# Kernel tuning notes

Measured on AMD Instinct MI355X. Metric: run time of the kernel, lower is better.

The kernel has to match this reference:

```python
import jax, jax.numpy as jnp
import numpy as np
from math import sqrt

N_BLOCKS = 15
N_HIDDEN = 128
N_BINARY = 10
NODE_DIM = 16
EDGE_DIM = 8
N_NODES = 20000
N_EDGES = 640000


def _norm_std(h):
    # x / x.std(-1, keepdim=True).detach()  (torch std is unbiased, ddof=1)
    s = jax.lax.stop_gradient(jnp.std(h, axis=-1, keepdims=True, ddof=1))
    return h / s


def setup_inputs() -> dict:
    key = jax.random.key(0)
    ks = jax.random.split(key, 16)
    inp = {
        "x": jax.random.uniform(ks[0], (N_NODES, NODE_DIM), jnp.float32),
        "edge_index": jax.random.randint(ks[1], (2, N_EDGES), 0, N_NODES, jnp.int32),
        "edge_attr": jax.random.uniform(ks[2], (N_EDGES, EDGE_DIM), jnp.float32),
        "embed_W": jax.random.normal(ks[3], (NODE_DIM, N_HIDDEN), jnp.float32) / sqrt(NODE_DIM),
        "embed_b": jax.random.normal(ks[4], (N_HIDDEN,), jnp.float32) * 0.02,
        "edge_W": jax.random.normal(ks[5], (N_BLOCKS, EDGE_DIM, N_HIDDEN), jnp.float32) / sqrt(EDGE_DIM),
        "edge_b": jax.random.normal(ks[6], (N_BLOCKS, N_HIDDEN), jnp.float32) * 0.02,
        "W1": jax.random.normal(ks[7], (N_BLOCKS, N_HIDDEN, N_HIDDEN), jnp.float32) / sqrt(N_HIDDEN),
        "b1": jax.random.normal(ks[8], (N_BLOCKS, N_HIDDEN), jnp.float32) * 0.02,
        "W2": jax.random.normal(ks[9], (N_BLOCKS, N_HIDDEN, N_HIDDEN), jnp.float32) / sqrt(N_HIDDEN),
        "b2": jax.random.normal(ks[10], (N_BLOCKS, N_HIDDEN), jnp.float32) * 0.02,
        "W3": jax.random.normal(ks[11], (N_BLOCKS, N_HIDDEN, N_HIDDEN), jnp.float32) / sqrt(N_HIDDEN),
        "b3": jax.random.normal(ks[12], (N_BLOCKS, N_HIDDEN), jnp.float32) * 0.02,
        "out_W": jax.random.normal(ks[13], (N_HIDDEN, N_BINARY), jnp.float32) / sqrt(N_HIDDEN),
        "out_b": jax.random.normal(ks[14], (N_BINARY,), jnp.float32) * 0.02,
    }
    return inp


def reference(x, edge_index, edge_attr, embed_W, embed_b, edge_W, edge_b,
              W1, b1, W2, b2, W3, b3, out_W, out_b):
    n_nodes = x.shape[0]
    src, dst = edge_index[0], edge_index[1]

    x = jnp.log(x + 1.0)                    # [N, node_dim]
    ea = jnp.log(edge_attr + 1.0)           # [E, edge_dim]
    h = x @ embed_W + embed_b               # [N, H]

    def block(h, p):
        eW, eb, w1, c1, w2, c2, w3, c3 = p
        x2 = _norm_std(h)
        e = ea @ eW + eb                    # per-block edge embedding [E, H]
        msg = jax.nn.relu(x2[src] + e)      # GINE message [E, H]
        agg = jax.ops.segment_sum(msg, dst, num_segments=n_nodes)  # [N, H]
        z = x2 + agg                        # (1 + eps) * x2 + aggr, eps=0
        z = jax.nn.relu(z @ w1 + c1)
        z = jax.nn.relu(z @ w2 + c2)
        z = z @ w3 + c3
        y = _norm_std(z)
        return h + y, None

    h, _ = jax.lax.scan(block, h, (edge_W, edge_b, W1, b1, W2, b2, W3, b3))

    h = h / sqrt(N_BLOCKS)
    logits = h @ out_W + out_b              # [N, N_BINARY]
    scale = 2.0 ** jnp.arange(N_BINARY, dtype=jnp.float32)  # fixed buffer
    return jnp.sum(logits * scale, axis=-1, keepdims=True)  # [N, 1]
```

## Files before the change

### kernel.cpp

```cpp
#include <hip/hip_runtime.h>
#include <hip/hip_bf16.h>
#include <hip/hip_fp16.h>

#define N_NODES 20000
#define N_EDGES 640000
#define N_HIDDEN 128
#define EDGE_DIM 8
#define NODE_DIM 16
#define N_BLOCKS 15
#define N_BINARY 10

typedef __attribute__((ext_vector_type(8))) _Float16 f16x8;
typedef __attribute__((ext_vector_type(4))) float f32x4;
typedef unsigned int uint;
typedef unsigned short ushort;

union U2H {
  uint u;
  __half2 h;
};
static __device__ __forceinline__ __half2 u2h2(uint u) {
  U2H c; c.u = u; return c.h;
}
static __device__ __forceinline__ ushort f2h_bits(float f) {
  union { _Float16 h; ushort u; } c;
  c.h = (_Float16)f;
  return c.u;
}

__global__ void k_embed(const float* __restrict__ x, const float* __restrict__ eW,
                        const float* __restrict__ ebias, float* __restrict__ h,
                        uint* __restrict__ x2p) {
  int wid = (blockIdx.x * blockDim.x + threadIdx.x) >> 6;
  int lane = threadIdx.x & 63;
  if (wid >= N_NODES) return;
  float xl[NODE_DIM];
#pragma unroll
  for (int k = 0; k < NODE_DIM; k++) xl[k] = logf(x[wid * NODE_DIM + k] + 1.0f);
  int c0 = lane, c1 = lane + 64;
  float h0 = ebias[c0], h1 = ebias[c1];
#pragma unroll
  for (int k = 0; k < NODE_DIM; k++) {
    h0 += xl[k] * eW[k * N_HIDDEN + c0];
    h1 += xl[k] * eW[k * N_HIDDEN + c1];
  }
  float ss = h0 + h1, s2 = h0 * h0 + h1 * h1;
#pragma unroll
  for (int m = 1; m < 64; m <<= 1) {
    ss += __shfl_xor(ss, m);
    s2 += __shfl_xor(s2, m);
  }
  float var = (s2 - ss * ss * (1.0f / 128.0f)) * (1.0f / 127.0f);
  float inv = 1.0f / sqrtf(var);
  size_t o = (size_t)wid * N_HIDDEN;
  h[o + c0] = h0;
  h[o + c1] = h1;
  uint pk = (uint)f2h_bits(h0 * inv) | ((uint)f2h_bits(h1 * inv) << 16);
  x2p[(size_t)wid * 64 + lane] = pk;
}

__global__ void k_count(const int* __restrict__ ei, int* __restrict__ deg,
                        int* __restrict__ rnk) {
  int e = blockIdx.x * blockDim.x + threadIdx.x;
  if (e < N_EDGES) rnk[e] = atomicAdd(&deg[ei[N_EDGES + e]], 1);
}

__global__ __launch_bounds__(1024) void k_scan(const int* __restrict__ deg,
                                               int* __restrict__ off) {
  __shared__ int wsum[16];
  int t = threadIdx.x;
  int lane = t & 63, w = t >> 6;
  int base = t * 20;
  int loc[20];
  int s = 0;
#pragma unroll
  for (int i = 0; i < 20; i++) {
    int idx = base + i;
    int d = (idx < N_NODES) ? deg[idx] : 0;
    loc[i] = s;
    s += d;
  }
  int incl = s;
#pragma unroll
  for (int m = 1; m < 64; m <<= 1) {
    int o = __shfl_up(incl, m);
    if (lane >= m) incl += o;
  }
  if (lane == 63) wsum[w] = incl;
  __syncthreads();
  if (w == 0) {
    int xv = (lane < 16) ? wsum[lane] : 0;
#pragma unroll
    for (int m = 1; m < 16; m <<= 1) {
      int o = __shfl_up(xv, m);
      if (lane >= m) xv += o;
    }
    if (lane < 16) wsum[lane] = xv;
  }
  __syncthreads();
  int woff = (w == 0) ? 0 : wsum[w - 1];
  int texcl = woff + incl - s;
#pragma unroll
  for (int i = 0; i < 20; i++) {
    int idx = base + i;
    if (idx < N_NODES) off[idx] = texcl + loc[i];
  }
  if (t == 0) off[N_NODES] = wsum[15];
}

__global__ void k_permute(const int* __restrict__ ei, const float* __restrict__ eattr,
                          const int* __restrict__ off, const int* __restrict__ rnk,
                          uint* __restrict__ srcoff, _Float16* __restrict__ ea_h) {
  int e = blockIdx.x * blockDim.x + threadIdx.x;
  if (e >= N_EDGES) return;
  int d = ei[N_EDGES + e];
  int pos = off[d] + rnk[e];
  srcoff[pos] = (uint)ei[e] * 64u;
  const float4* ap = (const float4*)(eattr + (size_t)e * 8);
  float4 a0 = ap[0], a1 = ap[1];
  f16x8 r;
  r[0] = (_Float16)logf(a0.x + 1.0f);
  r[1] = (_Float16)logf(a0.y + 1.0f);
  r[2] = (_Float16)logf(a0.z + 1.0f);
  r[3] = (_Float16)logf(a0.w + 1.0f);
  r[4] = (_Float16)logf(a1.x + 1.0f);
  r[5] = (_Float16)logf(a1.y + 1.0f);
  r[6] = (_Float16)logf(a1.z + 1.0f);
  r[7] = (_Float16)logf(a1.w + 1.0f);
  *(f16x8*)(ea_h + (size_t)pos * 8) = r;
}

__global__ void k_prep_w(const float* __restrict__ W1, const float* __restrict__ W2,
                         const float* __restrict__ W3, _Float16* __restrict__ Wt) {
  __shared__ _Float16 t[128][130];
  int m = blockIdx.x;
  int blk = m / 3, layer = m % 3;
  const float* src = (layer == 0 ? W1 : layer == 1 ? W2 : W3) + (size_t)blk * 16384;
  int tid = threadIdx.x;
  for (int idx = tid; idx < 16384; idx += 256) {
    int k = idx >> 7, n = idx & 127;
    t[k][n] = (_Float16)src[idx];
  }
  __syncthreads();
  _Float16* dst = Wt + (size_t)m * 16384;
  if (layer == 0) {
    for (int idx = tid; idx < 16384; idx += 256) {
      int n = idx >> 7, p = idx & 127;
      int k = (p >> 1) + 64 * (p & 1);
      dst[idx] = t[k][n];
    }
  } else {
    for (int idx = tid; idx < 16384; idx += 256) {
      int n = idx >> 7, k = idx & 127;
      dst[idx] = t[k][n];
    }
  }
}

__global__ __launch_bounds__(256) void k_block(
    const int* __restrict__ off, const uint* __restrict__ srcoff,
    const _Float16* __restrict__ ea_h, const uint* __restrict__ x2in,
    const float* __restrict__ eW, const float* __restrict__ ebias,
    const _Float16* __restrict__ Wt, const float* __restrict__ b1,
    const float* __restrict__ b2, const float* __restrict__ b3,
    float* __restrict__ h, uint* __restrict__ x2out) {
  __shared__ __align__(16) uint lzU[16 * 68];
  __shared__ float zf[16][132];
  int tid = threadIdx.x;
  int w = tid >> 6, lane = tid & 63;
  int l15 = lane & 15, g = lane >> 4;
  int g0 = blockIdx.x * 16;

  __half2 w0pk[4], w1pk[4];
#pragma unroll
  for (int j = 0; j < 4; j++) {
    w0pk[j] = __floats2half2_rn(eW[(2 * j) * N_HIDDEN + lane],
                                eW[(2 * j + 1) * N_HIDDEN + lane]);
    w1pk[j] = __floats2half2_rn(eW[(2 * j) * N_HIDDEN + lane + 64],
                                eW[(2 * j + 1) * N_HIDDEN + lane + 64]);
  }
  __half2 bb01 = __floats2half2_rn(ebias[lane], ebias[lane + 64]);

#define EDGE_COMPUTE(EV, UA)                                                   \
  {                                                                            \
    __half2 pA = __hmul2(u2h2((EV).x), w0pk[0]);                               \
    pA = __hfma2(u2h2((EV).y), w0pk[1], pA);                                   \
    pA = __hfma2(u2h2((EV).z), w0pk[2], pA);                                   \
    pA = __hfma2(u2h2((EV).w), w0pk[3], pA);                                   \
    __half2 pB = __hmul2(u2h2((EV).x), w1pk[0]);                               \
    pB = __hfma2(u2h2((EV).y), w1pk[1], pB);                                   \
    pB = __hfma2(u2h2((EV).z), w1pk[2], pB);                                   \
    pB = __hfma2(u2h2((EV).w), w1pk[3], pB);                                   \
    __half v0 = __hadd(__low2half(pA), __high2half(pA));                       \
    __half v1 = __hadd(__low2half(pB), __high2half(pB));                       \
    __half2 mm = __hadd2(__halves2half2(v0, v1), __hadd2(u2h2(UA), bb01));     \
    acc0 += fmaxf(__low2float(mm), 0.f);                                       \
    acc1 += fmaxf(__high2float(mm), 0.f);                                      \
  }
#define SLOAD4(SO, EV, EE)                                                     \
  {                                                                            \
    int eU_ = __builtin_amdgcn_readfirstlane(EE);                              \
    SO[0] = srcoff[eU_];                                                       \
    SO[1] = srcoff[eU_ + 1];                                                   \
    SO[2] = srcoff[eU_ + 2];                                                   \
    SO[3] = srcoff[eU_ + 3];                                                   \
    const uint4* ep_ = (const uint4*)(ea_h + (size_t)eU_ * 8);                 \
    EV[0] = ep_[0];                                                            \
    EV[1] = ep_[1];                                                            \
    EV[2] = ep_[2];                                                            \
    EV[3] = ep_[3];                                                            \
  }
#define GATHER4(UA, SO)                                                        \
  {                                                                            \
    UA[0] = x2in[SO[0] + lane];                                                \
    UA[1] = x2in[SO[1] + lane];                                                \
    UA[2] = x2in[SO[2] + lane];                                                \
    UA[3] = x2in[SO[3] + lane];                                                \
  }
#define COMP4(EV, UA)                                                          \
  {                                                                            \
    EDGE_COMPUTE(EV[0], UA[0]);                                                \
    EDGE_COMPUTE(EV[1], UA[1]);                                                \
    EDGE_COMPUTE(EV[2], UA[2]);                                                \
    EDGE_COMPUTE(EV[3], UA[3]);                                                \
  }

  for (int i = 0; i < 4; ++i) {
    int nl = w * 4 + i;
    int nU = __builtin_amdgcn_readfirstlane(g0 + nl);
    int eBeg = off[nU], eEnd = off[nU + 1];
    float acc0 = 0.f, acc1 = 0.f;

    uint soA[4], soB[4], uaA[4], uaB[4];
    uint4 evA[4], evB[4];
    int n4 = (eEnd - eBeg) >> 2;
    int e = eBeg;
    if (n4 > 0) {
      SLOAD4(soA, evA, e);
      SLOAD4(soB, evB, e + 4);
      GATHER4(uaA, soA);
      int gg = 0;
      for (; gg + 1 < n4; gg += 2) {
        GATHER4(uaB, soB);
        COMP4(evA, uaA);
        SLOAD4(soA, evA, e + 8);
        GATHER4(uaA, soA);
        COMP4(evB, uaB);
        SLOAD4(soB, evB, e + 12);
        e += 8;
      }
      if (gg < n4) {
        COMP4(evA, uaA);
        e += 4;
      }
    }
    for (; e < eEnd; ++e) {
      int eU = __builtin_amdgcn_readfirstlane(e);
      uint so = srcoff[eU];
      uint4 ev = *(const uint4*)(ea_h + (size_t)eU * 8);
      uint ua = x2in[so + lane];
      EDGE_COMPUTE(ev, ua);
    }

    uint xp = x2in[(uint)nU * 64u + lane];
    float z0 = __low2float(u2h2(xp)) + acc0;
    float z1 = __high2float(u2h2(xp)) + acc1;
    lzU[nl * 68 + lane] = (uint)f2h_bits(z0) | ((uint)f2h_bits(z1) << 16);
  }
#undef COMP4
#undef GATHER4
#undef SLOAD4
#undef EDGE_COMPUTE
  __syncthreads();

  f32x4 acc[2];
  f16x8 a[4];
  ushort* lzS = (ushort*)lzU;

#pragma unroll
  for (int kk = 0; kk < 4; kk++)
    a[kk] = *(const f16x8*)&lzU[l15 * 68 + kk * 16 + g * 4];
  __syncthreads();
#pragma unroll
  for (int c = 0; c < 2; c++) {
    float bv = b1[32 * w + c * 16 + l15];
    acc[c] = (f32x4){bv, bv, bv, bv};
  }
#pragma unroll
  for (int c = 0; c < 2; c++) {
    int col = 32 * w + c * 16 + l15;
#pragma unroll
    for (int kk = 0; kk < 4; kk++) {
      f16x8 bf = *(const f16x8*)(Wt + (size_t)col * 128 + kk * 32 + g * 8);
      acc[c] = __builtin_amdgcn_mfma_f32_16x16x32_f16(a[kk], bf, acc[c], 0, 0, 0);
    }
  }
#pragma unroll
  for (int c = 0; c < 2; c++)
#pragma unroll
    for (int r = 0; r < 4; r++)
      lzS[(4 * g + r) * 136 + 32 * w + c * 16 + l15] =
          f2h_bits(fmaxf(acc[c][r], 0.f));
  __syncthreads();

#pragma unroll
  for (int kk = 0; kk < 4; kk++)
    a[kk] = *(const f16x8*)&lzU[l15 * 68 + kk * 16 + g * 4];
  __syncthreads();
#pragma unroll
  for (int c = 0; c < 2; c++) {
    float bv = b2[32 * w + c * 16 + l15];
    acc[c] = (f32x4){bv, bv, bv, bv};
  }
  {
    const _Float16* W2t = Wt + 16384;
#pragma unroll
    for (int c = 0; c < 2; c++) {
      int col = 32 * w + c * 16 + l15;
#pragma unroll
      for (int kk = 0; kk < 4; kk++) {
        f16x8 bf = *(const f16x8*)(W2t + (size_t)col * 128 + kk * 32 + g * 8);
        acc[c] = __builtin_amdgcn_mfma_f32_16x16x32_f16(a[kk], bf, acc[c], 0, 0, 0);
      }
    }
  }
#pragma unroll
  for (int c = 0; c < 2; c++)
#pragma unroll
    for (int r = 0; r < 4; r++)
      lzS[(4 * g + r) * 136 + 32 * w + c * 16 + l15] =
          f2h_bits(fmaxf(acc[c][r], 0.f));
  __syncthreads();

#pragma unroll
  for (int kk = 0; kk < 4; kk++)
    a[kk] = *(const f16x8*)&lzU[l15 * 68 + kk * 16 + g * 4];
#pragma unroll
  for (int c = 0; c < 2; c++) {
    float bv = b3[32 * w + c * 16 + l15];
    acc[c] = (f32x4){bv, bv, bv, bv};
  }
  {
    const _Float16* W3t = Wt + 32768;
#pragma unroll
    for (int c = 0; c < 2; c++) {
      int col = 32 * w + c * 16 + l15;
#pragma unroll
      for (int kk = 0; kk < 4; kk++) {
        f16x8 bf = *(const f16x8*)(W3t + (size_t)col * 128 + kk * 32 + g * 8);
        acc[c] = __builtin_amdgcn_mfma_f32_16x16x32_f16(a[kk], bf, acc[c], 0, 0, 0);
      }
    }
  }
#pragma unroll
  for (int c = 0; c < 2; c++)
#pragma unroll
    for (int r = 0; r < 4; r++)
      zf[4 * g + r][32 * w + c * 16 + l15] = acc[c][r];
  __syncthreads();

#pragma unroll
  for (int i = 0; i < 4; ++i) {
    int nl = w * 4 + i;
    int n = g0 + nl;
    float z0 = zf[nl][lane], z1 = zf[nl][lane + 64];
    float ss = z0 + z1, s2 = z0 * z0 + z1 * z1;
#pragma unroll
    for (int m = 1; m < 64; m <<= 1) {
      ss += __shfl_xor(ss, m);
      s2 += __shfl_xor(s2, m);
    }
    float inv = 1.0f / sqrtf((s2 - ss * ss * (1.0f / 128.0f)) * (1.0f / 127.0f));
    size_t o = (size_t)n * 128;
    float h0 = h[o + lane] + z0 * inv;
    float h1 = h[o + lane + 64] + z1 * inv;
    float ts = h0 + h1, t2 = h0 * h0 + h1 * h1;
#pragma unroll
    for (int m = 1; m < 64; m <<= 1) {
      ts += __shfl_xor(ts, m);
      t2 += __shfl_xor(t2, m);
    }
    float inv2 = 1.0f / sqrtf((t2 - ts * ts * (1.0f / 128.0f)) * (1.0f / 127.0f));
    h[o + lane] = h0;
    h[o + lane + 64] = h1;
    uint pk = (uint)f2h_bits(h0 * inv2) | ((uint)f2h_bits(h1 * inv2) << 16);
    x2out[(uint)n * 64u + lane] = pk;
  }
}

__global__ void k_out(const float* __restrict__ h, const float* __restrict__ oW,
                      const float* __restrict__ ob, float* __restrict__ out) {
  int wid = (blockIdx.x * blockDim.x + threadIdx.x) >> 6;
  int lane = threadIdx.x & 63;
  if (wid >= N_NODES) return;
  int c0 = lane, c1 = lane + 64;
  float w0 = 0.f, w1 = 0.f, bsum = 0.f;
#pragma unroll
  for (int j = 0; j < N_BINARY; j++) {
    float sc = (float)(1 << j);
    w0 += oW[c0 * N_BINARY + j] * sc;
    w1 += oW[c1 * N_BINARY + j] * sc;
    bsum += ob[j] * sc;
  }
  size_t o = (size_t)wid * 128;
  float v = h[o + c0] * w0 + h[o + c1] * w1;
#pragma unroll
  for (int m = 1; m < 64; m <<= 1) v += __shfl_xor(v, m);
  if (lane == 0) out[wid] = v * (1.0f / sqrtf(15.0f)) + bsum;
}

extern "C" void kernel_launch(void* const* d_in, const int* in_sizes, int n_in,
                              void* d_out, int out_size, void* d_ws, size_t ws_size,
                              hipStream_t stream) {
  const float* x = (const float*)d_in[0];
  const int* ei = (const int*)d_in[1];
  const float* eattr = (const float*)d_in[2];
  const float* embW = (const float*)d_in[3];
  const float* embB = (const float*)d_in[4];
  const float* edgeW = (const float*)d_in[5];
  const float* edgeB = (const float*)d_in[6];
  const float* W1 = (const float*)d_in[7];
  const float* b1 = (const float*)d_in[8];
  const float* W2 = (const float*)d_in[9];
  const float* b2 = (const float*)d_in[10];
  const float* W3 = (const float*)d_in[11];
  const float* b3 = (const float*)d_in[12];
  const float* outW = (const float*)d_in[13];
  const float* outB = (const float*)d_in[14];
  float* out = (float*)d_out;

  char* base = (char*)d_ws;
  size_t o = 0;
  auto carve = [&](size_t bytes) {
    size_t start = o;
    o = (start + bytes + 255) & ~(size_t)255;
    return (void*)(base + start);
  };
  int* deg = (int*)carve(N_NODES * sizeof(int));
  int* off = (int*)carve((N_NODES + 1) * sizeof(int));
  int* rnk = (int*)carve(N_EDGES * sizeof(int));
  uint* srcoff = (uint*)carve((N_EDGES + 16) * sizeof(uint));
  _Float16* ea_h = (_Float16*)carve((size_t)(N_EDGES + 16) * EDGE_DIM * 2);
  uint* x2a = (uint*)carve((size_t)N_NODES * 64 * sizeof(uint));
  uint* x2b = (uint*)carve((size_t)N_NODES * 64 * sizeof(uint));
  float* h = (float*)carve((size_t)N_NODES * N_HIDDEN * sizeof(float));
  _Float16* Wt = (_Float16*)carve((size_t)45 * 16384 * 2);

  hipMemsetAsync(deg, 0, N_NODES * sizeof(int), stream);
  hipMemsetAsync(srcoff + N_EDGES, 0, 16 * sizeof(uint), stream);
  k_embed<<<N_NODES / 4, 256, 0, stream>>>(x, embW, embB, h, x2a);
  k_count<<<(N_EDGES + 255) / 256, 256, 0, stream>>>(ei, deg, rnk);
  k_scan<<<1, 1024, 0, stream>>>(deg, off);
  k_permute<<<(N_EDGES + 255) / 256, 256, 0, stream>>>(ei, eattr, off, rnk, srcoff, ea_h);
  k_prep_w<<<45, 256, 0, stream>>>(W1, W2, W3, Wt);

  for (int b = 0; b < N_BLOCKS; b++) {
    const uint* x2i = (b & 1) ? x2b : x2a;
    uint* x2o = (b & 1) ? x2a : x2b;
    k_block<<<N_NODES / 16, 256, 0, stream>>>(
        off, srcoff, ea_h, x2i, edgeW + (size_t)b * EDGE_DIM * N_HIDDEN,
        edgeB + (size_t)b * N_HIDDEN, Wt + (size_t)b * 3 * 16384,
        b1 + (size_t)b * N_HIDDEN, b2 + (size_t)b * N_HIDDEN,
        b3 + (size_t)b * N_HIDDEN, h, x2o);
  }
  k_out<<<N_NODES / 4, 256, 0, stream>>>(h, outW, outB, out);
}
```

Measured before the change: 957.2 us.

## Use eight waves per block to halve per-wave node and column work

Each k_block workgroup now launches 512 threads (8 waves) instead of 256. Each wave gathers edges for 2 nodes instead of 4 and computes one 16-column MFMA tile per layer instead of two. The goal is more concurrent waves hiding the latency of the irregular gather, plus shorter serial chains per wave. In exchange, the register budget per thread is tighter under the 512 launch bound, and each workgroup has more waves meeting at every barrier.

```diff
diff --git a/kernel.cpp b/kernel.cpp
--- a/kernel.cpp
+++ b/kernel.cpp
@@ -157,7 +157,7 @@
   }
 }
 
-__global__ __launch_bounds__(256) void k_block(
+__global__ __launch_bounds__(512) void k_block(
     const int* __restrict__ off, const uint* __restrict__ srcoff,
     const _Float16* __restrict__ ea_h, const uint* __restrict__ x2in,
     const float* __restrict__ eW, const float* __restrict__ ebias,
@@ -225,8 +225,8 @@
     EDGE_COMPUTE(EV[3], UA[3]);                                                \
   }
 
-  for (int i = 0; i < 4; ++i) {
-    int nl = w * 4 + i;
+  for (int i = 0; i < 2; ++i) {
+    int nl = w * 2 + i;
     int nU = __builtin_amdgcn_readfirstlane(g0 + nl);
     int eBeg = off[nU], eEnd = off[nU + 1];
     float acc0 = 0.f, acc1 = 0.f;
@@ -273,95 +273,68 @@
 #undef EDGE_COMPUTE
   __syncthreads();
 
-  f32x4 acc[2];
+  f32x4 acc;
   f16x8 a[4];
   ushort* lzS = (ushort*)lzU;
+  int col = 16 * w + l15;
 
 #pragma unroll
   for (int kk = 0; kk < 4; kk++)
     a[kk] = *(const f16x8*)&lzU[l15 * 68 + kk * 16 + g * 4];
   __syncthreads();
-#pragma unroll
-  for (int c = 0; c < 2; c++) {
-    float bv = b1[32 * w + c * 16 + l15];
-    acc[c] = (f32x4){bv, bv, bv, bv};
-  }
-#pragma unroll
-  for (int c = 0; c < 2; c++) {
-    int col = 32 * w + c * 16 + l15;
+  {
+    float bv = b1[col];
+    acc = (f32x4){bv, bv, bv, bv};
 #pragma unroll
     for (int kk = 0; kk < 4; kk++) {
       f16x8 bf = *(const f16x8*)(Wt + (size_t)col * 128 + kk * 32 + g * 8);
-      acc[c] = __builtin_amdgcn_mfma_f32_16x16x32_f16(a[kk], bf, acc[c], 0, 0, 0);
-    }
-  }
-#pragma unroll
-  for (int c = 0; c < 2; c++)
-#pragma unroll
-    for (int r = 0; r < 4; r++)
-      lzS[(4 * g + r) * 136 + 32 * w + c * 16 + l15] =
-          f2h_bits(fmaxf(acc[c][r], 0.f));
+      acc = __builtin_amdgcn_mfma_f32_16x16x32_f16(a[kk], bf, acc, 0, 0, 0);
+    }
+  }
+#pragma unroll
+  for (int r = 0; r < 4; r++)
+    lzS[(4 * g + r) * 136 + col] = f2h_bits(fmaxf(acc[r], 0.f));
   __syncthreads();
 
 #pragma unroll
   for (int kk = 0; kk < 4; kk++)
     a[kk] = *(const f16x8*)&lzU[l15 * 68 + kk * 16 + g * 4];
   __syncthreads();
-#pragma unroll
-  for (int c = 0; c < 2; c++) {
-    float bv = b2[32 * w + c * 16 + l15];
-    acc[c] = (f32x4){bv, bv, bv, bv};
-  }
   {
     const _Float16* W2t = Wt + 16384;
-#pragma unroll
-    for (int c = 0; c < 2; c++) {
-      int col = 32 * w + c * 16 + l15;
-#pragma unroll
-      for (int kk = 0; kk < 4; kk++) {
-        f16x8 bf = *(const f16x8*)(W2t + (size_t)col * 128 + kk * 32 + g * 8);
-        acc[c] = __builtin_amdgcn_mfma_f32_16x16x32_f16(a[kk], bf, acc[c], 0, 0, 0);
-      }
-    }
-  }
-#pragma unroll
-  for (int c = 0; c < 2; c++)
-#pragma unroll
-    for (int r = 0; r < 4; r++)
-      lzS[(4 * g + r) * 136 + 32 * w + c * 16 + l15] =
-          f2h_bits(fmaxf(acc[c][r], 0.f));
+    float bv = b2[col];
+    acc = (f32x4){bv, bv, bv, bv};
+#pragma unroll
+    for (int kk = 0; kk < 4; kk++) {
+      f16x8 bf = *(const f16x8*)(W2t + (size_t)col * 128 + kk * 32 + g * 8);
+      acc = __builtin_amdgcn_mfma_f32_16x16x32_f16(a[kk], bf, acc, 0, 0, 0);
+    }
+  }
+#pragma unroll
+  for (int r = 0; r < 4; r++)
+    lzS[(4 * g + r) * 136 + col] = f2h_bits(fmaxf(acc[r], 0.f));
   __syncthreads();
 
 #pragma unroll
   for (int kk = 0; kk < 4; kk++)
     a[kk] = *(const f16x8*)&lzU[l15 * 68 + kk * 16 + g * 4];
-#pragma unroll
-  for (int c = 0; c < 2; c++) {
-    float bv = b3[32 * w + c * 16 + l15];
-    acc[c] = (f32x4){bv, bv, bv, bv};
-  }
   {
     const _Float16* W3t = Wt + 32768;
-#pragma unroll
-    for (int c = 0; c < 2; c++) {
-      int col = 32 * w + c * 16 + l15;
-#pragma unroll
-      for (int kk = 0; kk < 4; kk++) {
-        f16x8 bf = *(const f16x8*)(W3t + (size_t)col * 128 + kk * 32 + g * 8);
-        acc[c] = __builtin_amdgcn_mfma_f32_16x16x32_f16(a[kk], bf, acc[c], 0, 0, 0);
-      }
-    }
-  }
-#pragma unroll
-  for (int c = 0; c < 2; c++)
-#pragma unroll
-    for (int r = 0; r < 4; r++)
-      zf[4 * g + r][32 * w + c * 16 + l15] = acc[c][r];
-  __syncthreads();
-
-#pragma unroll
-  for (int i = 0; i < 4; ++i) {
-    int nl = w * 4 + i;
+    float bv = b3[col];
+    acc = (f32x4){bv, bv, bv, bv};
+#pragma unroll
+    for (int kk = 0; kk < 4; kk++) {
+      f16x8 bf = *(const f16x8*)(W3t + (size_t)col * 128 + kk * 32 + g * 8);
+      acc = __builtin_amdgcn_mfma_f32_16x16x32_f16(a[kk], bf, acc, 0, 0, 0);
+    }
+  }
+#pragma unroll
+  for (int r = 0; r < 4; r++) zf[4 * g + r][col] = acc[r];
+  __syncthreads();
+
+#pragma unroll
+  for (int i = 0; i < 2; ++i) {
+    int nl = w * 2 + i;
     int n = g0 + nl;
     float z0 = zf[nl][lane], z1 = zf[nl][lane + 64];
     float ss = z0 + z1, s2 = z0 * z0 + z1 * z1;
@@ -457,7 +430,7 @@
   for (int b = 0; b < N_BLOCKS; b++) {
     const uint* x2i = (b & 1) ? x2b : x2a;
     uint* x2o = (b & 1) ? x2a : x2b;
-    k_block<<<N_NODES / 16, 256, 0, stream>>>(
+    k_block<<<N_NODES / 16, 512, 0, stream>>>(
         off, srcoff, ea_h, x2i, edgeW + (size_t)b * EDGE_DIM * N_HIDDEN,
         edgeB + (size_t)b * N_HIDDEN, Wt + (size_t)b * 3 * 16384,
         b1 + (size_t)b * N_HIDDEN, b2 + (size_t)b * N_HIDDEN,
```

New measurement: 885.9 us. 7.5% less time.
